# Performance work log

Hardware: AMD Instinct MI355X
Metric: run time of the kernel (lower is better)

## Reference

```python
import jax, jax.numpy as jnp
import numpy as np

B, K, D, H = 32768, 16, 256, 2
HD = D // H
LN_EPS = 1e-5


def setup_inputs() -> dict:
    key = jax.random.key(0)
    ks = jax.random.split(key, 10)
    s = 1.0 / np.sqrt(D)
    return {
        "center_emb": jax.random.normal(ks[0], (B, D), dtype=jnp.float32),
        "neighbor_embs": jax.random.normal(ks[1], (B, K, D), dtype=jnp.float32),
        "edge_weights": jax.random.uniform(ks[2], (B, K), dtype=jnp.float32),
        "Wq": jax.random.uniform(ks[3], (D, D), jnp.float32, -s, s),
        "Wk": jax.random.uniform(ks[4], (D, D), jnp.float32, -s, s),
        "Wv": jax.random.uniform(ks[5], (D, D), jnp.float32, -s, s),
        "Wc": jax.random.uniform(ks[6], (D // 2, D), jnp.float32, -s, s),
        "Wx": jax.random.uniform(ks[7], (D // 2, D), jnp.float32, -s, s),
        "ln_gamma": jnp.ones((D,), jnp.float32),
        "ln_beta": jnp.zeros((D,), jnp.float32),
    }


def reference(center_emb, neighbor_embs, edge_weights, Wq, Wk, Wv, Wc, Wx, ln_gamma, ln_beta):
    scale = HD ** -0.5
    # projections (nn.Linear: x @ W.T)
    q = (center_emb @ Wq.T).reshape(B, H, HD)          # [B,H,hd]
    k = (neighbor_embs @ Wk.T).reshape(B, K, H, HD)    # [B,K,H,hd]
    v = (neighbor_embs @ Wv.T).reshape(B, K, H, HD)
    # attention scores with additive edge-weight topology bias
    scores = jnp.einsum("bhd,bkhd->bhk", q, k) * scale + edge_weights[:, None, :]
    attn = jax.nn.softmax(scores, axis=-1)             # [B,H,K] (dropout: eval mode)
    context = jnp.einsum("bhk,bkhd->bhd", attn, v).reshape(B, D)
    # LayerNorm over D
    mu = jnp.mean(context, axis=-1, keepdims=True)
    var = jnp.var(context, axis=-1, keepdims=True)
    ctx_n = (context - mu) * jax.lax.rsqrt(var + LN_EPS) * ln_gamma + ln_beta
    # concat of center / context half-projections
    return jnp.concatenate([center_emb @ Wc.T, ctx_n @ Wx.T], axis=-1)
```

## Files before the change

kernel.cpp:

```cpp
#include <hip/hip_runtime.h>

#define Bsz 32768
#define BR  32
#define SCALE 0.08838834764831845f

typedef __attribute__((ext_vector_type(4))) float f32x4;
typedef __attribute__((ext_vector_type(4))) unsigned short us4;
typedef __attribute__((ext_vector_type(4))) unsigned int ui4;
typedef __attribute__((ext_vector_type(2))) unsigned int ui2;
typedef _Float16 __attribute__((ext_vector_type(2))) h2;

static __device__ __forceinline__ unsigned int pk16(float a, float b){
  return __builtin_bit_cast(unsigned int, __builtin_amdgcn_cvt_pkrtz(a, b));
}
static __device__ __forceinline__ h2 uph(unsigned int u){
  return __builtin_bit_cast(h2, u);
}
static __device__ __forceinline__ float h2f(unsigned short h){
  return (float)__builtin_bit_cast(_Float16, h);
}
#define FDOT2(a, b, c) __builtin_amdgcn_fdot2((a), (b), (c), false)

__global__ void prep_kernel(const float* __restrict__ Wq, const float* __restrict__ Wk,
                            const float* __restrict__ Wv, const float* __restrict__ Wc,
                            const float* __restrict__ Wx, unsigned int* __restrict__ wsp){
  unsigned int* W1P = wsp;
  unsigned int* W2P = wsp + 128*640;
  unsigned int* W3P = W2P + 128*256;
  const int n = blockIdx.x;
  const int k = threadIdx.x;
  float val;
  if (n < 512){
    const int h = n >> 8, m = n & 255;
    const float* wq = Wq + h*128*256 + k;
    const float* wk = Wk + h*128*256 + m;
    float s = 0.f;
    for (int d = 0; d < 128; ++d) s += wq[d*256] * wk[d*256];
    val = s;
  } else if (n < 640){
    val = Wc[(n-512)*256 + k];
  } else if (n < 896){
    val = Wv[(n-640)*256 + k];
  } else {
    val = Wx[(n-896)*256 + k];
  }
  const float vo = __shfl_xor(val, 1, 64);
  if ((k & 1) == 0){
    const unsigned int p = pk16(val, vo);
    const int kp = k >> 1;
    if (n < 640)      W1P[kp*640 + n] = p;
    else if (n < 896) W2P[kp*256 + (n-640)] = p;
    else              W3P[kp*128 + (n-896)] = p;
  }
}

__global__ __launch_bounds__(256, 4) void fused_kernel(
    const float* __restrict__ center, const float* __restrict__ nbr,
    const float* __restrict__ ew, const float* __restrict__ gamma,
    const float* __restrict__ beta, const unsigned int* __restrict__ Wall,
    float* __restrict__ out)
{
  __shared__ __align__(16) unsigned short s_ctil[BR*520];

  const int tid  = threadIdx.x;
  const int wid  = tid >> 6;
  const int lane = tid & 63;
  const int b0   = blockIdx.x * BR;

  const unsigned int* W1P = Wall;
  const unsigned int* W2P = Wall + 128*640;
  const unsigned int* W3P = W2P + 128*256;

  const int rt = tid >> 5;
  const int ct = tid & 31;

  {
    const int sr = tid >> 3;
    const int fc = (tid & 7) * 32;
    const float* cp = center + ((long)(b0 + sr) << 8) + fc;
    #pragma unroll
    for (int it = 0; it < 4; ++it){
      float4 a = *(const float4*)(cp + it*8);
      float4 b = *(const float4*)(cp + it*8 + 4);
      ui4 v = {pk16(a.x,a.y), pk16(a.z,a.w), pk16(b.x,b.y), pk16(b.z,b.w)};
      *(ui4*)&s_ctil[sr*520 + 256 + fc + it*8] = v;
    }
  }

  {
    f32x4 acc[4][3];
    #pragma unroll
    for (int rr = 0; rr < 4; ++rr)
      #pragma unroll
      for (int t = 0; t < 3; ++t) acc[rr][t] = (f32x4){0,0,0,0};
    #pragma unroll 1
    for (int k0 = 0; k0 < 256; k0 += 8){
      ui4 a8[4];
      #pragma unroll
      for (int rr = 0; rr < 4; ++rr)
        a8[rr] = *(const ui4*)&s_ctil[(4*rt+rr)*520 + 256 + k0];
      #pragma unroll
      for (int kp = 0; kp < 4; ++kp){
        const unsigned int* wrow = W1P + ((k0>>1) + kp)*640;
        const ui4 w0 = ((const ui4*)(wrow      ))[ct];
        const ui4 w1 = ((const ui4*)(wrow + 128))[ct];
        const ui4 w4 = ((const ui4*)(wrow + 512))[ct];
        #pragma unroll
        for (int rr = 0; rr < 4; ++rr){
          const h2 a2 = uph(a8[rr][kp]);
          #pragma unroll
          for (int j = 0; j < 4; ++j){
            acc[rr][0][j] = FDOT2(a2, uph(w0[j]), acc[rr][0][j]);
            acc[rr][1][j] = FDOT2(a2, uph(w1[j]), acc[rr][1][j]);
            acc[rr][2][j] = FDOT2(a2, uph(w4[j]), acc[rr][2][j]);
          }
        }
      }
    }
    #pragma unroll
    for (int rr = 0; rr < 4; ++rr){
      const int r = 4*rt + rr;
      ui2 v0 = {pk16(acc[rr][0][0], acc[rr][0][1]), pk16(acc[rr][0][2], acc[rr][0][3])};
      ui2 v1 = {pk16(acc[rr][1][0], acc[rr][1][1]), pk16(acc[rr][1][2], acc[rr][1][3])};
      *(ui2*)&s_ctil[r*520 + ct*4]       = v0;
      *(ui2*)&s_ctil[r*520 + 128 + ct*4] = v1;
      *(f32x4*)&out[((long)(b0 + r) << 8) + ct*4] = acc[rr][2];
    }
  }

  {
    f32x4 acc[4][2];
    #pragma unroll
    for (int rr = 0; rr < 4; ++rr){ acc[rr][0] = (f32x4){0,0,0,0}; acc[rr][1] = (f32x4){0,0,0,0}; }
    #pragma unroll 1
    for (int k0 = 0; k0 < 256; k0 += 8){
      ui4 a8[4];
      #pragma unroll
      for (int rr = 0; rr < 4; ++rr)
        a8[rr] = *(const ui4*)&s_ctil[(4*rt+rr)*520 + 256 + k0];
      #pragma unroll
      for (int kp = 0; kp < 4; ++kp){
        const unsigned int* wrow = W1P + ((k0>>1) + kp)*640;
        const ui4 w2 = ((const ui4*)(wrow + 256))[ct];
        const ui4 w3 = ((const ui4*)(wrow + 384))[ct];
        #pragma unroll
        for (int rr = 0; rr < 4; ++rr){
          const h2 a2 = uph(a8[rr][kp]);
          #pragma unroll
          for (int j = 0; j < 4; ++j){
            acc[rr][0][j] = FDOT2(a2, uph(w2[j]), acc[rr][0][j]);
            acc[rr][1][j] = FDOT2(a2, uph(w3[j]), acc[rr][1][j]);
          }
        }
      }
    }
    #pragma unroll
    for (int rr = 0; rr < 4; ++rr){
      const int r = 4*rt + rr;
      ui2 v0 = {pk16(acc[rr][0][0], acc[rr][0][1]), pk16(acc[rr][0][2], acc[rr][0][3])};
      ui2 v1 = {pk16(acc[rr][1][0], acc[rr][1][1]), pk16(acc[rr][1][2], acc[rr][1][3])};
      *(ui2*)&s_ctil[r*520 + 256 + ct*4] = v0;
      *(ui2*)&s_ctil[r*520 + 384 + ct*4] = v1;
    }
  }

  {
    const int myk = ((lane>>4)&1)*8 + ((lane>>3)&1)*4 + ((lane>>2)&1)*2 + ((lane>>1)&1);
    const int myh = lane >> 5;
    #pragma unroll 1
    for (int rr = 0; rr < 8; ++rr){
      const int r = wid*8 + rr;
      const long b = b0 + r;
      float4 c0, c1;
      {
        us4 h0 = *(const us4*)&s_ctil[r*520 + lane*4];
        us4 h1 = *(const us4*)&s_ctil[r*520 + 256 + lane*4];
        c0.x=h2f(h0[0]); c0.y=h2f(h0[1]); c0.z=h2f(h0[2]); c0.w=h2f(h0[3]);
        c1.x=h2f(h1[0]); c1.y=h2f(h1[1]); c1.z=h2f(h1[2]); c1.w=h2f(h1[3]);
      }
      float4 xv[16];
      const float* npt = nbr + ((b << 4) << 8) + lane*4;
      #pragma unroll
      for (int k = 0; k < 16; ++k) xv[k] = *(const float4*)(npt + (k << 8));
      float P0[16], P1[16];
      #pragma unroll
      for (int k = 0; k < 16; ++k){
        P0[k] = xv[k].x*c0.x + xv[k].y*c0.y + xv[k].z*c0.z + xv[k].w*c0.w;
        P1[k] = xv[k].x*c1.x + xv[k].y*c1.y + xv[k].z*c1.z + xv[k].w*c1.w;
      }
      const int b5 = lane & 32, b4 = lane & 16, b3 = lane & 8, b2 = lane & 4, b1 = lane & 2;
      float Q[16];
      #pragma unroll
      for (int j = 0; j < 16; ++j){
        const float give = b5 ? P0[j] : P1[j];
        const float keep = b5 ? P1[j] : P0[j];
        Q[j] = keep + __shfl_xor(give, 32, 64);
      }
      float R[8];
      #pragma unroll
      for (int j = 0; j < 8; ++j){
        const float give = b4 ? Q[j] : Q[8+j];
        const float keep = b4 ? Q[8+j] : Q[j];
        R[j] = keep + __shfl_xor(give, 16, 64);
      }
      float S[4];
      #pragma unroll
      for (int j = 0; j < 4; ++j){
        const float give = b3 ? R[j] : R[4+j];
        const float keep = b3 ? R[4+j] : R[j];
        S[j] = keep + __shfl_xor(give, 8, 64);
      }
      float T[2];
      #pragma unroll
      for (int j = 0; j < 2; ++j){
        const float give = b2 ? S[j] : S[2+j];
        const float keep = b2 ? S[2+j] : S[j];
        T[j] = keep + __shfl_xor(give, 4, 64);
      }
      float U;
      {
        const float give = b1 ? T[0] : T[1];
        const float keep = b1 ? T[1] : T[0];
        U = keep + __shfl_xor(give, 2, 64);
      }
      const float sfull = U + __shfl_xor(U, 1, 64);
      const float erk = ew[b*16 + myk];
      const float e = __expf(sfull*SCALE + erk);
      float dn = e;
      dn += __shfl_xor(dn, 2, 64);
      dn += __shfl_xor(dn, 4, 64);
      dn += __shfl_xor(dn, 8, 64);
      dn += __shfl_xor(dn, 16, 64);
      const float w = e / dn;
      float* wbuf = (float*)&s_ctil[r*520 + 256];
      wbuf[myh*16 + myk] = w;
      f32x4 wv[8];
      #pragma unroll
      for (int t = 0; t < 8; ++t) wv[t] = ((const f32x4*)wbuf)[t];
      float4 agg0 = {0,0,0,0}, agg1 = {0,0,0,0};
      #pragma unroll
      for (int k = 0; k < 16; ++k){
        const float w0 = wv[k>>2][k&3];
        const float w1 = wv[4 + (k>>2)][k&3];
        agg0.x += w0*xv[k].x; agg0.y += w0*xv[k].y; agg0.z += w0*xv[k].z; agg0.w += w0*xv[k].w;
        agg1.x += w1*xv[k].x; agg1.y += w1*xv[k].y; agg1.z += w1*xv[k].z; agg1.w += w1*xv[k].w;
      }
      ui2 v0 = {pk16(agg0.x, agg0.y), pk16(agg0.z, agg0.w)};
      ui2 v1 = {pk16(agg1.x, agg1.y), pk16(agg1.z, agg1.w)};
      *(ui2*)&s_ctil[r*520 + lane*4]       = v0;
      *(ui2*)&s_ctil[r*520 + 256 + lane*4] = v1;
    }
  }

  {
    f32x4 cacc[4][2];
    #pragma unroll
    for (int rr = 0; rr < 4; ++rr){ cacc[rr][0] = (f32x4){0,0,0,0}; cacc[rr][1] = (f32x4){0,0,0,0}; }
    #pragma unroll 1
    for (int k0 = 0; k0 < 256; k0 += 8){
      ui4 a0[4], a1[4];
      #pragma unroll
      for (int rr = 0; rr < 4; ++rr){
        a0[rr] = *(const ui4*)&s_ctil[(4*rt+rr)*520 + k0];
        a1[rr] = *(const ui4*)&s_ctil[(4*rt+rr)*520 + 256 + k0];
      }
      #pragma unroll
      for (int kp = 0; kp < 4; ++kp){
        const unsigned int* wrow = W2P + ((k0>>1) + kp)*256;
        const ui4 w0 = ((const ui4*)(wrow      ))[ct];
        const ui4 w1 = ((const ui4*)(wrow + 128))[ct];
        #pragma unroll
        for (int rr = 0; rr < 4; ++rr){
          const h2 x0 = uph(a0[rr][kp]);
          const h2 x1 = uph(a1[rr][kp]);
          #pragma unroll
          for (int j = 0; j < 4; ++j){
            cacc[rr][0][j] = FDOT2(x0, uph(w0[j]), cacc[rr][0][j]);
            cacc[rr][1][j] = FDOT2(x1, uph(w1[j]), cacc[rr][1][j]);
          }
        }
      }
    }
    const f32x4 gv0 = ((const f32x4*)gamma)[ct], gv1 = ((const f32x4*)gamma)[32 + ct];
    const f32x4 bv0 = ((const f32x4*)beta )[ct], bv1 = ((const f32x4*)beta )[32 + ct];
    #pragma unroll
    for (int rr = 0; rr < 4; ++rr){
      float s = 0.f, q = 0.f;
      #pragma unroll
      for (int t = 0; t < 2; ++t)
        #pragma unroll
        for (int j = 0; j < 4; ++j){
          const float x = cacc[rr][t][j];
          s += x; q += x*x;
        }
      #pragma unroll
      for (int m = 16; m >= 1; m >>= 1){
        s += __shfl_xor(s, m, 64);
        q += __shfl_xor(q, m, 64);
      }
      const float mu  = s * (1.f/256.f);
      const float var = q * (1.f/256.f) - mu*mu;
      const float rs  = rsqrtf(var + 1e-5f);
      const int r = 4*rt + rr;
      float y0[4], y1[4];
      #pragma unroll
      for (int j = 0; j < 4; ++j){
        y0[j] = (cacc[rr][0][j] - mu)*rs*gv0[j] + bv0[j];
        y1[j] = (cacc[rr][1][j] - mu)*rs*gv1[j] + bv1[j];
      }
      ui2 v0 = {pk16(y0[0], y0[1]), pk16(y0[2], y0[3])};
      ui2 v1 = {pk16(y1[0], y1[1]), pk16(y1[2], y1[3])};
      *(ui2*)&s_ctil[r*520 + ct*4]       = v0;
      *(ui2*)&s_ctil[r*520 + 128 + ct*4] = v1;
    }
  }

  {
    f32x4 eacc[4];
    #pragma unroll
    for (int rr = 0; rr < 4; ++rr) eacc[rr] = (f32x4){0,0,0,0};
    #pragma unroll 1
    for (int k0 = 0; k0 < 256; k0 += 8){
      ui4 a[4];
      #pragma unroll
      for (int rr = 0; rr < 4; ++rr)
        a[rr] = *(const ui4*)&s_ctil[(4*rt+rr)*520 + k0];
      #pragma unroll
      for (int kp = 0; kp < 4; ++kp){
        const ui4 w = ((const ui4*)(W3P + ((k0>>1) + kp)*128))[ct];
        #pragma unroll
        for (int rr = 0; rr < 4; ++rr){
          const h2 x = uph(a[rr][kp]);
          #pragma unroll
          for (int j = 0; j < 4; ++j)
            eacc[rr][j] = FDOT2(x, uph(w[j]), eacc[rr][j]);
        }
      }
    }
    #pragma unroll
    for (int rr = 0; rr < 4; ++rr)
      *(f32x4*)&out[((long)(b0 + 4*rt + rr) << 8) + 128 + ct*4] = eacc[rr];
  }
}

extern "C" void kernel_launch(void* const* d_in, const int* in_sizes, int n_in,
                              void* d_out, int out_size, void* d_ws, size_t ws_size,
                              hipStream_t stream){
  const float* center = (const float*)d_in[0];
  const float* nbr    = (const float*)d_in[1];
  const float* ew     = (const float*)d_in[2];
  const float* Wq     = (const float*)d_in[3];
  const float* Wk     = (const float*)d_in[4];
  const float* Wv     = (const float*)d_in[5];
  const float* Wc     = (const float*)d_in[6];
  const float* Wx     = (const float*)d_in[7];
  const float* gamma  = (const float*)d_in[8];
  const float* beta   = (const float*)d_in[9];
  (void)in_sizes; (void)n_in; (void)out_size;

  unsigned int* W = (unsigned int*)d_ws;
  (void)ws_size;

  prep_kernel<<<1024, 256, 0, stream>>>(Wq, Wk, Wv, Wc, Wx, W);
  fused_kernel<<<Bsz/BR, 256, 0, stream>>>(center, nbr, ew, gamma, beta, W, (float*)d_out);
}
```

Before: 254.2 us.

## Split fused kernel into center-projection and neighbor-attention kernels

Splits the single fused kernel into two. The first computes the center-side projections (folded q·Wk and q·Wv tiles plus the Wc output half) and writes them as fp16 to a workspace buffer. The second handles the attention over neighbors, LayerNorm and the output projection with 16-row, 128-thread blocks and a smaller shared-memory footprint. The aim is to let each phase run at its own occupancy and to shrink the working set of the bandwidth-bound neighbor phase. The cost is an extra launch and a global round trip for the intermediate tiles.

Measured after the change: 300.7 us. 1.18x slower.

```diff
diff --git a/kernel.cpp b/kernel.cpp
--- a/kernel.cpp
+++ b/kernel.cpp
@@ -1,7 +1,6 @@
 #include <hip/hip_runtime.h>
 
 #define Bsz 32768
-#define BR  32
 #define SCALE 0.08838834764831845f
 
 typedef __attribute__((ext_vector_type(4))) float f32x4;
@@ -54,23 +53,15 @@
   }
 }
 
-__global__ __launch_bounds__(256, 4) void fused_kernel(
-    const float* __restrict__ center, const float* __restrict__ nbr,
-    const float* __restrict__ ew, const float* __restrict__ gamma,
-    const float* __restrict__ beta, const unsigned int* __restrict__ Wall,
-    float* __restrict__ out)
+__global__ __launch_bounds__(256, 4) void a_kernel(
+    const float* __restrict__ center, const unsigned int* __restrict__ Wall,
+    unsigned int* __restrict__ ctileu, float* __restrict__ out)
 {
-  __shared__ __align__(16) unsigned short s_ctil[BR*520];
-
-  const int tid  = threadIdx.x;
-  const int wid  = tid >> 6;
-  const int lane = tid & 63;
-  const int b0   = blockIdx.x * BR;
-
+  __shared__ __align__(16) unsigned short s_c[32*264];
+
+  const int tid = threadIdx.x;
+  const int b0  = blockIdx.x * 32;
   const unsigned int* W1P = Wall;
-  const unsigned int* W2P = Wall + 128*640;
-  const unsigned int* W3P = W2P + 128*256;
-
   const int rt = tid >> 5;
   const int ct = tid & 31;
 
@@ -83,7 +74,7 @@
       float4 a = *(const float4*)(cp + it*8);
       float4 b = *(const float4*)(cp + it*8 + 4);
       ui4 v = {pk16(a.x,a.y), pk16(a.z,a.w), pk16(b.x,b.y), pk16(b.z,b.w)};
-      *(ui4*)&s_ctil[sr*520 + 256 + fc + it*8] = v;
+      *(ui4*)&s_c[sr*264 + fc + it*8] = v;
     }
   }
 
@@ -98,7 +89,7 @@
       ui4 a8[4];
       #pragma unroll
       for (int rr = 0; rr < 4; ++rr)
-        a8[rr] = *(const ui4*)&s_ctil[(4*rt+rr)*520 + 256 + k0];
+        a8[rr] = *(const ui4*)&s_c[(4*rt+rr)*264 + k0];
       #pragma unroll
       for (int kp = 0; kp < 4; ++kp){
         const unsigned int* wrow = W1P + ((k0>>1) + kp)*640;
@@ -119,12 +110,12 @@
     }
     #pragma unroll
     for (int rr = 0; rr < 4; ++rr){
-      const int r = 4*rt + rr;
+      const long r = b0 + 4*rt + rr;
       ui2 v0 = {pk16(acc[rr][0][0], acc[rr][0][1]), pk16(acc[rr][0][2], acc[rr][0][3])};
       ui2 v1 = {pk16(acc[rr][1][0], acc[rr][1][1]), pk16(acc[rr][1][2], acc[rr][1][3])};
-      *(ui2*)&s_ctil[r*520 + ct*4]       = v0;
-      *(ui2*)&s_ctil[r*520 + 128 + ct*4] = v1;
-      *(f32x4*)&out[((long)(b0 + r) << 8) + ct*4] = acc[rr][2];
+      *(ui2*)&ctileu[r*256 +      ct*2] = v0;
+      *(ui2*)&ctileu[r*256 + 64 + ct*2] = v1;
+      *(f32x4*)&out[(r << 8) + ct*4] = acc[rr][2];
     }
   }
 
@@ -137,7 +128,7 @@
       ui4 a8[4];
       #pragma unroll
       for (int rr = 0; rr < 4; ++rr)
-        a8[rr] = *(const ui4*)&s_ctil[(4*rt+rr)*520 + 256 + k0];
+        a8[rr] = *(const ui4*)&s_c[(4*rt+rr)*264 + k0];
       #pragma unroll
       for (int kp = 0; kp < 4; ++kp){
         const unsigned int* wrow = W1P + ((k0>>1) + kp)*640;
@@ -156,13 +147,33 @@
     }
     #pragma unroll
     for (int rr = 0; rr < 4; ++rr){
-      const int r = 4*rt + rr;
+      const long r = b0 + 4*rt + rr;
       ui2 v0 = {pk16(acc[rr][0][0], acc[rr][0][1]), pk16(acc[rr][0][2], acc[rr][0][3])};
       ui2 v1 = {pk16(acc[rr][1][0], acc[rr][1][1]), pk16(acc[rr][1][2], acc[rr][1][3])};
-      *(ui2*)&s_ctil[r*520 + 256 + ct*4] = v0;
-      *(ui2*)&s_ctil[r*520 + 384 + ct*4] = v1;
-    }
-  }
+      *(ui2*)&ctileu[r*256 + 128 + ct*2] = v0;
+      *(ui2*)&ctileu[r*256 + 192 + ct*2] = v1;
+    }
+  }
+}
+
+__global__ __launch_bounds__(128, 4) void b_kernel(
+    const float* __restrict__ nbr, const float* __restrict__ ew,
+    const float* __restrict__ gamma, const float* __restrict__ beta,
+    const unsigned int* __restrict__ Wall, const unsigned int* __restrict__ ctileu,
+    float* __restrict__ out)
+{
+  __shared__ __align__(16) unsigned short s2[16*520];
+
+  const int tid  = threadIdx.x;
+  const int wid  = tid >> 6;
+  const int lane = tid & 63;
+  const int b0   = blockIdx.x * 16;
+
+  const unsigned int* W2P = Wall + 128*640;
+  const unsigned int* W3P = W2P + 128*256;
+
+  const int rt = tid >> 5;
+  const int ct = lane & 31;
 
   {
     const int myk = ((lane>>4)&1)*8 + ((lane>>3)&1)*4 + ((lane>>2)&1)*2 + ((lane>>1)&1);
@@ -173,10 +184,11 @@
       const long b = b0 + r;
       float4 c0, c1;
       {
-        us4 h0 = *(const us4*)&s_ctil[r*520 + lane*4];
-        us4 h1 = *(const us4*)&s_ctil[r*520 + 256 + lane*4];
-        c0.x=h2f(h0[0]); c0.y=h2f(h0[1]); c0.z=h2f(h0[2]); c0.w=h2f(h0[3]);
-        c1.x=h2f(h1[0]); c1.y=h2f(h1[1]); c1.z=h2f(h1[2]); c1.w=h2f(h1[3]);
+        ui2 u0 = *(const ui2*)&ctileu[b*256 + lane*2];
+        ui2 u1 = *(const ui2*)&ctileu[b*256 + 128 + lane*2];
+        h2 p0 = uph(u0[0]), p1 = uph(u0[1]), p2 = uph(u1[0]), p3 = uph(u1[1]);
+        c0.x=(float)p0[0]; c0.y=(float)p0[1]; c0.z=(float)p1[0]; c0.w=(float)p1[1];
+        c1.x=(float)p2[0]; c1.y=(float)p2[1]; c1.z=(float)p3[0]; c1.w=(float)p3[1];
       }
       float4 xv[16];
       const float* npt = nbr + ((b << 4) << 8) + lane*4;
@@ -232,7 +244,7 @@
       dn += __shfl_xor(dn, 8, 64);
       dn += __shfl_xor(dn, 16, 64);
       const float w = e / dn;
-      float* wbuf = (float*)&s_ctil[r*520 + 256];
+      float* wbuf = (float*)&s2[r*520 + 256];
       wbuf[myh*16 + myk] = w;
       f32x4 wv[8];
       #pragma unroll
@@ -247,8 +259,8 @@
       }
       ui2 v0 = {pk16(agg0.x, agg0.y), pk16(agg0.z, agg0.w)};
       ui2 v1 = {pk16(agg1.x, agg1.y), pk16(agg1.z, agg1.w)};
-      *(ui2*)&s_ctil[r*520 + lane*4]       = v0;
-      *(ui2*)&s_ctil[r*520 + 256 + lane*4] = v1;
+      *(ui2*)&s2[r*520 + lane*4]       = v0;
+      *(ui2*)&s2[r*520 + 256 + lane*4] = v1;
     }
   }
 
@@ -261,8 +273,8 @@
       ui4 a0[4], a1[4];
       #pragma unroll
       for (int rr = 0; rr < 4; ++rr){
-        a0[rr] = *(const ui4*)&s_ctil[(4*rt+rr)*520 + k0];
-        a1[rr] = *(const ui4*)&s_ctil[(4*rt+rr)*520 + 256 + k0];
+        a0[rr] = *(const ui4*)&s2[(4*rt+rr)*520 + k0];
+        a1[rr] = *(const ui4*)&s2[(4*rt+rr)*520 + 256 + k0];
       }
       #pragma unroll
       for (int kp = 0; kp < 4; ++kp){
@@ -310,8 +322,8 @@
       }
       ui2 v0 = {pk16(y0[0], y0[1]), pk16(y0[2], y0[3])};
       ui2 v1 = {pk16(y1[0], y1[1]), pk16(y1[2], y1[3])};
-      *(ui2*)&s_ctil[r*520 + ct*4]       = v0;
-      *(ui2*)&s_ctil[r*520 + 128 + ct*4] = v1;
+      *(ui2*)&s2[r*520 + ct*4]       = v0;
+      *(ui2*)&s2[r*520 + 128 + ct*4] = v1;
     }
   }
 
@@ -321,16 +333,16 @@
     for (int rr = 0; rr < 4; ++rr) eacc[rr] = (f32x4){0,0,0,0};
     #pragma unroll 1
     for (int k0 = 0; k0 < 256; k0 += 8){
-      ui4 a[4];
+      ui4 a8[4];
       #pragma unroll
       for (int rr = 0; rr < 4; ++rr)
-        a[rr] = *(const ui4*)&s_ctil[(4*rt+rr)*520 + k0];
+        a8[rr] = *(const ui4*)&s2[(4*rt+rr)*520 + k0];
       #pragma unroll
       for (int kp = 0; kp < 4; ++kp){
         const ui4 w = ((const ui4*)(W3P + ((k0>>1) + kp)*128))[ct];
         #pragma unroll
         for (int rr = 0; rr < 4; ++rr){
-          const h2 x = uph(a[rr][kp]);
+          const h2 x = uph(a8[rr][kp]);
           #pragma unroll
           for (int j = 0; j < 4; ++j)
             eacc[rr][j] = FDOT2(x, uph(w[j]), eacc[rr][j]);
@@ -358,9 +370,11 @@
   const float* beta   = (const float*)d_in[9];
   (void)in_sizes; (void)n_in; (void)out_size;
 
-  unsigned int* W = (unsigned int*)d_ws;
+  unsigned int* W  = (unsigned int*)d_ws;
+  unsigned int* CT = W + 131072;
   (void)ws_size;
 
   prep_kernel<<<1024, 256, 0, stream>>>(Wq, Wk, Wv, Wc, Wx, W);
-  fused_kernel<<<Bsz/BR, 256, 0, stream>>>(center, nbr, ew, gamma, beta, W, (float*)d_out);
-}
+  a_kernel<<<Bsz/32, 256, 0, stream>>>(center, W, CT, (float*)d_out);
+  b_kernel<<<Bsz/16, 128, 0, stream>>>(nbr, ew, gamma, beta, W, CT, (float*)d_out);
+}
```

## Prefetch next row's neighbor tile and use fp16 dot2 for score products

Applied to the files above, without the earlier changes.

Loads the 16x256 neighbor slab for the next batch row in the middle of the current row's shuffle reduction, software-pipelining the dominant global reads across rows. The current row's values are first packed to fp16 and the score dot products use fdot2 instead of fp32 FMAs. The weighted aggregation then reads these fp16-packed values. This trades extra registers (two copies of the tile) and some precision for hiding load latency and fewer ALU ops.

After: 294.7 us. +16.0%, slower.

```diff
diff --git a/kernel.cpp b/kernel.cpp
--- a/kernel.cpp
+++ b/kernel.cpp
@@ -15,9 +15,6 @@
 }
 static __device__ __forceinline__ h2 uph(unsigned int u){
   return __builtin_bit_cast(h2, u);
-}
-static __device__ __forceinline__ float h2f(unsigned short h){
-  return (float)__builtin_bit_cast(_Float16, h);
 }
 #define FDOT2(a, b, c) __builtin_amdgcn_fdot2((a), (b), (c), false)
 
@@ -167,26 +164,30 @@
   {
     const int myk = ((lane>>4)&1)*8 + ((lane>>3)&1)*4 + ((lane>>2)&1)*2 + ((lane>>1)&1);
     const int myh = lane >> 5;
+    float4 xv[16];
+    {
+      const float* npt0 = nbr + (((long)(b0 + wid*8)) << 12) + lane*4;
+      #pragma unroll
+      for (int k = 0; k < 16; ++k) xv[k] = *(const float4*)(npt0 + (k << 8));
+    }
     #pragma unroll 1
     for (int rr = 0; rr < 8; ++rr){
       const int r = wid*8 + rr;
       const long b = b0 + r;
-      float4 c0, c1;
-      {
-        us4 h0 = *(const us4*)&s_ctil[r*520 + lane*4];
-        us4 h1 = *(const us4*)&s_ctil[r*520 + 256 + lane*4];
-        c0.x=h2f(h0[0]); c0.y=h2f(h0[1]); c0.z=h2f(h0[2]); c0.w=h2f(h0[3]);
-        c1.x=h2f(h1[0]); c1.y=h2f(h1[1]); c1.z=h2f(h1[2]); c1.w=h2f(h1[3]);
-      }
-      float4 xv[16];
-      const float* npt = nbr + ((b << 4) << 8) + lane*4;
-      #pragma unroll
-      for (int k = 0; k < 16; ++k) xv[k] = *(const float4*)(npt + (k << 8));
+      ui2 u0 = *(const ui2*)&s_ctil[r*520 + lane*4];
+      ui2 u1 = *(const ui2*)&s_ctil[r*520 + 256 + lane*4];
+      const h2 c00 = uph(u0[0]), c01 = uph(u0[1]);
+      const h2 c10 = uph(u1[0]), c11 = uph(u1[1]);
+      ui2 xvp[16];
+      #pragma unroll
+      for (int k = 0; k < 16; ++k)
+        xvp[k] = (ui2){pk16(xv[k].x, xv[k].y), pk16(xv[k].z, xv[k].w)};
       float P0[16], P1[16];
       #pragma unroll
       for (int k = 0; k < 16; ++k){
-        P0[k] = xv[k].x*c0.x + xv[k].y*c0.y + xv[k].z*c0.z + xv[k].w*c0.w;
-        P1[k] = xv[k].x*c1.x + xv[k].y*c1.y + xv[k].z*c1.z + xv[k].w*c1.w;
+        const h2 xa = uph(xvp[k][0]), xb = uph(xvp[k][1]);
+        P0[k] = FDOT2(xb, c01, FDOT2(xa, c00, 0.f));
+        P1[k] = FDOT2(xb, c11, FDOT2(xa, c10, 0.f));
       }
       const int b5 = lane & 32, b4 = lane & 16, b3 = lane & 8, b2 = lane & 4, b1 = lane & 2;
       float Q[16];
@@ -202,6 +203,11 @@
         const float give = b4 ? Q[j] : Q[8+j];
         const float keep = b4 ? Q[8+j] : Q[j];
         R[j] = keep + __shfl_xor(give, 16, 64);
+      }
+      if (rr < 7){
+        const float* nptn = nbr + ((b + 1) << 12) + lane*4;
+        #pragma unroll
+        for (int k = 0; k < 16; ++k) xv[k] = *(const float4*)(nptn + (k << 8));
       }
       float S[4];
       #pragma unroll
@@ -242,8 +248,11 @@
       for (int k = 0; k < 16; ++k){
         const float w0 = wv[k>>2][k&3];
         const float w1 = wv[4 + (k>>2)][k&3];
-        agg0.x += w0*xv[k].x; agg0.y += w0*xv[k].y; agg0.z += w0*xv[k].z; agg0.w += w0*xv[k].w;
-        agg1.x += w1*xv[k].x; agg1.y += w1*xv[k].y; agg1.z += w1*xv[k].z; agg1.w += w1*xv[k].w;
+        const h2 pa = uph(xvp[k][0]), pb = uph(xvp[k][1]);
+        const float x0 = (float)pa[0], x1 = (float)pa[1];
+        const float x2 = (float)pb[0], x3 = (float)pb[1];
+        agg0.x += w0*x0; agg0.y += w0*x1; agg0.z += w0*x2; agg0.w += w0*x3;
+        agg1.x += w1*x0; agg1.y += w1*x1; agg1.z += w1*x2; agg1.w += w1*x3;
       }
       ui2 v0 = {pk16(agg0.x, agg0.y), pk16(agg0.z, agg0.w)};
       ui2 v1 = {pk16(agg1.x, agg1.y), pk16(agg1.z, agg1.w)};
@@ -321,16 +330,16 @@
     for (int rr = 0; rr < 4; ++rr) eacc[rr] = (f32x4){0,0,0,0};
     #pragma unroll 1
     for (int k0 = 0; k0 < 256; k0 += 8){
-      ui4 a[4];
+      ui4 a8[4];
       #pragma unroll
       for (int rr = 0; rr < 4; ++rr)
-        a[rr] = *(const ui4*)&s_ctil[(4*rt+rr)*520 + k0];
+        a8[rr] = *(const ui4*)&s_ctil[(4*rt+rr)*520 + k0];
       #pragma unroll
       for (int kp = 0; kp < 4; ++kp){
         const ui4 w = ((const ui4*)(W3P + ((k0>>1) + kp)*128))[ct];
         #pragma unroll
         for (int rr = 0; rr < 4; ++rr){
-          const h2 x = uph(a[rr][kp]);
+          const h2 x = uph(a8[rr][kp]);
           #pragma unroll
           for (int j = 0; j < 4; ++j)
             eacc[rr][j] = FDOT2(x, uph(w[j]), eacc[rr][j]);
```
